# Performance work log

Measured on AMD Instinct MI355X. Metric: run time of the kernel, lower is better.

Reference implementation:

```python
import jax, jax.numpy as jnp
import numpy as np

NUM_BINS = 256
EPS = 1e-8


def setup_inputs() -> dict:
    key = jax.random.key(0)
    k1, k2 = jax.random.split(key)
    x = jax.random.uniform(k1, (4096, 8192), dtype=jnp.float32)
    y = jax.random.uniform(k2, (4096, 8192), dtype=jnp.float32)
    return {"x": x, "y": y}


def reference(x, y):
    # min-max normalize to [0, 1]
    xn = (x - jnp.min(x)) / (jnp.max(x) - jnp.min(x) + EPS)
    yn = (y - jnp.min(y)) / (jnp.max(y) - jnp.min(y) + EPS)
    # bin indices, clamped to [0, NUM_BINS-1] (floor(1.0*N) == N gets clipped)
    x_idx = jnp.clip(jnp.floor(xn * NUM_BINS).astype(jnp.int32), 0, NUM_BINS - 1)
    y_idx = jnp.clip(jnp.floor(yn * NUM_BINS).astype(jnp.int32), 0, NUM_BINS - 1)
    n = x.shape[0] * x.shape[1]
    # joint histogram via scatter-add on flattened (x_idx, y_idx) pairs
    flat = (x_idx * NUM_BINS + y_idx).reshape(-1)
    hist_xy = jnp.zeros((NUM_BINS * NUM_BINS,), jnp.float32).at[flat].add(1.0)
    hist_xy = hist_xy.reshape(NUM_BINS, NUM_BINS)
    p_xy = hist_xy / n
    p_x = jnp.sum(p_xy, axis=1)  # marginal over y
    p_y = jnp.sum(p_xy, axis=0)  # marginal over x
    # MI: sum over cells where p_xy>0 and both marginals>0
    px_py = p_x[:, None] * p_y[None, :]
    valid = (p_xy > 0) & (p_x[:, None] > 0) & (p_y[None, :] > 0)
    safe_pxy = jnp.where(valid, p_xy, 1.0)
    safe_den = jnp.where(valid, px_py, 1.0)
    mi = jnp.sum(jnp.where(valid, p_xy * jnp.log(safe_pxy / safe_den), 0.0))
    # normalized MI
    h_x = -jnp.sum(p_x * jnp.log(p_x + EPS))
    h_y = -jnp.sum(p_y * jnp.log(p_y + EPS))
    mi = mi / (jnp.sqrt(h_x * h_y) + EPS)
    return -mi
```

## Files before the change

kernel.cpp:

```cpp
#include <hip/hip_runtime.h>
#include <stdint.h>
#include <math.h>

#define HIST_BINS   65536
#define HIST_WORDS8 16384

typedef float f4 __attribute__((ext_vector_type(4)));

__device__ __forceinline__ f4 ldnt(const f4* p){ return __builtin_nontemporal_load(p); }

__device__ __forceinline__ uint32_t f2key(float f){
    uint32_t u = __float_as_uint(f);
    return (u & 0x80000000u) ? ~u : (u | 0x80000000u);
}
__device__ __forceinline__ float key2f(uint32_t k){
    uint32_t u = (k & 0x80000000u) ? (k ^ 0x80000000u) : ~k;
    return __uint_as_float(u);
}


__global__ void init_kernel(uint32_t* __restrict__ mm, uint32_t* __restrict__ csum){
    int t = threadIdx.x;
    if (t < 4) mm[t] = (t & 1) ? 0u : 0xFFFFFFFFu;
    csum[t] = 0u;
}

__device__ __forceinline__ void mm4(f4 a, float& mn, float& mx){
    mn = fminf(mn, fminf(fminf(a[0], a[1]), fminf(a[2], a[3])));
    mx = fmaxf(mx, fmaxf(fmaxf(a[0], a[1]), fmaxf(a[2], a[3])));
}

__global__ void __launch_bounds__(1024)
minmax_kernel(const f4* __restrict__ x, const f4* __restrict__ y,
              uint32_t* __restrict__ mm, int n4, int nblk_per){
    int isy = (blockIdx.x >= (unsigned)nblk_per) ? 1 : 0;
    const f4* __restrict__ src = isy ? y : x;
    int bid = blockIdx.x - isy * nblk_per;
    int seg = n4 / nblk_per;
    int base = bid * seg;
    const int chunk = 1024 * 8;
    float mn = INFINITY, mx = -INFINITY;
    int off = 0;
    for (; off + chunk <= seg; off += chunk){
        const f4* p = src + base + off + threadIdx.x;
        f4 v0 = p[0],        v1 = p[1024],     v2 = p[2 * 1024], v3 = p[3 * 1024];
        f4 v4 = p[4 * 1024], v5 = p[5 * 1024], v6 = p[6 * 1024], v7 = p[7 * 1024];
        mm4(v0, mn, mx); mm4(v1, mn, mx); mm4(v2, mn, mx); mm4(v3, mn, mx);
        mm4(v4, mn, mx); mm4(v5, mn, mx); mm4(v6, mn, mx); mm4(v7, mn, mx);
    }
    for (int i = base + off + threadIdx.x; i < base + seg; i += 1024) mm4(src[i], mn, mx);
    if (bid == nblk_per - 1)
        for (int i = nblk_per * seg + threadIdx.x; i < n4; i += 1024) mm4(src[i], mn, mx);

    #pragma unroll
    for (int o = 32; o > 0; o >>= 1){
        mn = fminf(mn, __shfl_down(mn, o, 64));
        mx = fmaxf(mx, __shfl_down(mx, o, 64));
    }
    __shared__ float smn[16], smx[16];
    int lane = threadIdx.x & 63, wid = threadIdx.x >> 6;
    if (lane == 0){ smn[wid] = mn; smx[wid] = mx; }
    __syncthreads();
    if (threadIdx.x == 0){
        for (int w = 1; w < 16; ++w){ mn = fminf(mn, smn[w]); mx = fmaxf(mx, smx[w]); }
        atomicMin(&mm[isy * 2 + 0], f2key(mn));
        atomicMax(&mm[isy * 2 + 1], f2key(mx));
    }
}

__device__ __forceinline__ void bin_pair(float vx, float vy,
                                         float mnx, float sx, float mny, float sy,
                                         uint32_t* lh){
    int ix = (int)floorf((vx - mnx) * sx);
    int iy = (int)floorf((vy - mny) * sy);
    ix = ix < 0 ? 0 : (ix > 255 ? 255 : ix);
    iy = iy < 0 ? 0 : (iy > 255 ? 255 : iy);
    uint32_t bin = ((uint32_t)ix << 8) | (uint32_t)iy;
    atomicAdd(&lh[bin >> 2], 1u << ((bin & 3u) * 8u));
}

__device__ __forceinline__ void bin4(f4 a, f4 b,
                                     float mnx, float sx, float mny, float sy,
                                     uint32_t* lh){
    bin_pair(a[0], b[0], mnx, sx, mny, sy, lh);
    bin_pair(a[1], b[1], mnx, sx, mny, sy, lh);
    bin_pair(a[2], b[2], mnx, sx, mny, sy, lh);
    bin_pair(a[3], b[3], mnx, sx, mny, sy, lh);
}

__global__ void __launch_bounds__(1024)
hist_kernel(const f4* __restrict__ x, const f4* __restrict__ y,
            const uint32_t* __restrict__ mm, uint32_t* __restrict__ out32,
            int n4, int atomic_flush){
    __shared__ uint32_t lh[HIST_WORDS8];
    for (int w = threadIdx.x; w < HIST_WORDS8; w += blockDim.x) lh[w] = 0u;
    __syncthreads();

    float mnx = key2f(mm[0]);
    float sx  = 256.0f / ((key2f(mm[1]) - mnx) + 1e-8f);
    float mny = key2f(mm[2]);
    float sy  = 256.0f / ((key2f(mm[3]) - mny) + 1e-8f);

    int seg  = n4 / gridDim.x;
    int base = blockIdx.x * seg;
    const int chunk = 1024 * 4;
    int off = 0;
    for (; off + chunk <= seg; off += chunk){
        const f4* px = x + base + off + threadIdx.x;
        const f4* py = y + base + off + threadIdx.x;
        f4 a0 = ldnt(px),            a1 = ldnt(px + 1024);
        f4 a2 = ldnt(px + 2 * 1024), a3 = ldnt(px + 3 * 1024);
        f4 b0 = ldnt(py),            b1 = ldnt(py + 1024);
        f4 b2 = ldnt(py + 2 * 1024), b3 = ldnt(py + 3 * 1024);
        bin4(a0, b0, mnx, sx, mny, sy, lh);
        bin4(a1, b1, mnx, sx, mny, sy, lh);
        bin4(a2, b2, mnx, sx, mny, sy, lh);
        bin4(a3, b3, mnx, sx, mny, sy, lh);
    }
    for (int i = base + off + threadIdx.x; i < base + seg; i += 1024)
        bin4(x[i], y[i], mnx, sx, mny, sy, lh);
    if (blockIdx.x == gridDim.x - 1)
        for (int i = gridDim.x * seg + threadIdx.x; i < n4; i += 1024)
            bin4(x[i], y[i], mnx, sx, mny, sy, lh);
    __syncthreads();

    if (!atomic_flush){
        uint32_t* part = out32 + (size_t)blockIdx.x * HIST_WORDS8;
        for (int w = threadIdx.x; w < HIST_WORDS8; w += blockDim.x) part[w] = lh[w];
    } else {
        for (int w = threadIdx.x; w < HIST_WORDS8; w += blockDim.x){
            uint32_t v = lh[w];
            if (v){
                uint32_t c0 = v & 255u, c1 = (v >> 8) & 255u, c2 = (v >> 16) & 255u, c3 = v >> 24;
                if (c0) atomicAdd(&out32[4*w + 0], c0);
                if (c1) atomicAdd(&out32[4*w + 1], c1);
                if (c2) atomicAdd(&out32[4*w + 2], c2);
                if (c3) atomicAdd(&out32[4*w + 3], c3);
            }
        }
    }
}

__global__ void __launch_bounds__(1024)
reduce_kernel(const uint32_t* __restrict__ partials, uint32_t* __restrict__ hist,
              uint32_t* __restrict__ rsum, uint32_t* __restrict__ csum, int nparts){
    __shared__ uint32_t sm[64][16][16];
    int t = threadIdx.x;
    int ql = t & 15, g = t >> 4;
    int per = nparts >> 6;
    uint32_t c[16];
    #pragma unroll
    for (int k = 0; k < 16; ++k) c[k] = 0;
    const uint4* base = (const uint4*)partials;
    size_t qoff = (size_t)blockIdx.x * 16 + ql;
    #pragma unroll 8
    for (int j = 0; j < per; ++j){
        uint4 v = base[(size_t)(g * per + j) * (HIST_WORDS8 / 4) + qoff];
        c[ 0] += v.x & 255u; c[ 1] += (v.x >> 8) & 255u; c[ 2] += (v.x >> 16) & 255u; c[ 3] += v.x >> 24;
        c[ 4] += v.y & 255u; c[ 5] += (v.y >> 8) & 255u; c[ 6] += (v.y >> 16) & 255u; c[ 7] += v.y >> 24;
        c[ 8] += v.z & 255u; c[ 9] += (v.z >> 8) & 255u; c[10] += (v.z >> 16) & 255u; c[11] += v.z >> 24;
        c[12] += v.w & 255u; c[13] += (v.w >> 8) & 255u; c[14] += (v.w >> 16) & 255u; c[15] += v.w >> 24;
    }
    #pragma unroll
    for (int k = 0; k < 16; ++k) sm[g][k][ql] = c[k];
    __syncthreads();
    uint32_t s = 0;
    if (t < 256){
        int q2 = t & 15;
        int k  = t >> 4;
        #pragma unroll 8
        for (int gg = 0; gg < 64; ++gg) s += sm[gg][k][q2];
        hist[(size_t)blockIdx.x * 256 + q2 * 16 + k] = s;
        atomicAdd(&csum[q2 * 16 + k], s);
    }
    __syncthreads();
    uint32_t* flat = &sm[0][0][0];
    if (t < 256){
        uint32_t bs = s;
        #pragma unroll
        for (int o = 32; o > 0; o >>= 1) bs += __shfl_down(bs, o, 64);
        if ((t & 63) == 0) flat[t >> 6] = bs;
    }
    __syncthreads();
    if (t == 0) rsum[blockIdx.x] = flat[0] + flat[1] + flat[2] + flat[3];
}

__device__ double bsum1024(double v, double* red, int t){
    #pragma unroll
    for (int o = 32; o > 0; o >>= 1) v += __shfl_down(v, o, 64);
    __syncthreads();
    if ((t & 63) == 0) red[t >> 6] = v;
    __syncthreads();
    if (t == 0){
        double s = 0.0;
        for (int w = 0; w < 16; ++w) s += red[w];
        v = s;
    }
    return v;
}

__global__ void __launch_bounds__(1024)
finalize_kernel(const uint32_t* __restrict__ hist,
                const uint32_t* __restrict__ rsum, const uint32_t* __restrict__ csum,
                float* __restrict__ out, int n, int marg){
    __shared__ uint32_t lrs[256], lcs[256];
    __shared__ uint32_t csum4[4][256];
    __shared__ double red[16];
    int t = threadIdx.x;

    if (!marg){
        if (t < 256){ lrs[t] = rsum[t]; lcs[t] = csum[t]; }
    } else {
        {
            int r = t >> 2, q = t & 3;
            const uint4* hp = (const uint4*)(hist + r * 256 + q * 64);
            uint32_t s = 0;
            #pragma unroll
            for (int k = 0; k < 16; ++k){ uint4 v = hp[k]; s += v.x + v.y + v.z + v.w; }
            s += __shfl_down(s, 2, 64);
            s += __shfl_down(s, 1, 64);
            if (q == 0) lrs[r] = s;
        }
        {
            int c = t & 255, g = t >> 8;
            const uint32_t* hp = hist + g * 64 * 256 + c;
            uint32_t s = 0;
            #pragma unroll 8
            for (int r = 0; r < 64; ++r) s += hp[r * 256];
            csum4[g][c] = s;
        }
        __syncthreads();
        if (t < 256) lcs[t] = csum4[0][t] + csum4[1][t] + csum4[2][t] + csum4[3][t];
    }
    __syncthreads();

    const double invn = 1.0 / (double)n;
    const double dn = (double)n;

    double mi = 0.0;
    {
        int q = t & 63, g = t >> 6;
        const uint4* h4 = (const uint4*)hist;
        for (int k = 0; k < 16; ++k){
            int r = g * 16 + k;
            uint4 v = h4[r * 64 + q];
            double rs = (double)lrs[r];
            uint32_t cc[4] = {v.x, v.y, v.z, v.w};
            #pragma unroll
            for (int j = 0; j < 4; ++j){
                if (cc[j]){
                    double ratio = ((double)cc[j] * dn) / (rs * (double)lcs[q * 4 + j]);
                    mi += (double)cc[j] * (double)logf((float)ratio);
                }
            }
        }
        mi *= invn;
    }
    double hx = 0.0, hy = 0.0;
    if (t < 256){
        double px = (double)lrs[t] * invn;
        double py = (double)lcs[t] * invn;
        hx = px * log(px + 1e-8);
        hy = py * log(py + 1e-8);
    }
    double mi_s = bsum1024(mi, red, t);
    double hx_s = bsum1024(hx, red, t);
    double hy_s = bsum1024(hy, red, t);
    if (t == 0){
        double h_x = -hx_s, h_y = -hy_s;
        double nmi = mi_s / (sqrt(h_x * h_y) + 1e-8);
        out[0] = (float)(-nmi);
    }
}

extern "C" void kernel_launch(void* const* d_in, const int* in_sizes, int n_in,
                              void* d_out, int out_size, void* d_ws, size_t ws_size,
                              hipStream_t stream){
    const f4* x = (const f4*)d_in[0];
    const f4* y = (const f4*)d_in[1];
    float* out = (float*)d_out;
    uint32_t* ws = (uint32_t*)d_ws;
    uint32_t* hist = ws;
    uint32_t* mm   = ws + HIST_BINS;
    uint32_t* rsum = ws + HIST_BINS + 64;
    uint32_t* csum = ws + HIST_BINS + 64 + 256;
    uint32_t* partials = ws + HIST_BINS + 64 + 512;

    int n  = in_sizes[0];
    int n4 = n / 4;

    size_t head = (size_t)HIST_BINS + 64 + 512;
    size_t need512 = (head + (size_t)512 * HIST_WORDS8) * 4;
    size_t need256 = (head + (size_t)256 * HIST_WORDS8) * 4;
    int nblk, atomic_flush;
    if (ws_size >= need512)      { nblk = 512; atomic_flush = 0; }
    else if (ws_size >= need256) { nblk = 256; atomic_flush = 0; }
    else                         { nblk = 512; atomic_flush = 1; }

    if (atomic_flush)
        hipMemsetAsync(hist, 0, HIST_BINS * sizeof(uint32_t), stream);
    init_kernel<<<1, 256, 0, stream>>>(mm, csum);
    minmax_kernel<<<512, 1024, 0, stream>>>(x, y, mm, n4, 256);
    hist_kernel<<<nblk, 1024, 0, stream>>>(x, y, mm,
                                           atomic_flush ? hist : partials, n4, atomic_flush);
    if (!atomic_flush)
        reduce_kernel<<<256, 1024, 0, stream>>>(partials, hist, rsum, csum, nblk);
    finalize_kernel<<<1, 1024, 0, stream>>>(hist, rsum, csum, out, n, atomic_flush);
}
```

Measured before the change: 371.3 us.

## Fuse reduce and finalize into cooperative kernel, drop init and atomic minmax

Per-block min/max results now go to slots and are reduced inside the histogram kernel, so the init kernel and the global atomics are gone. The reduce and finalize kernels merge into one cooperative kernel that uses grid syncs for the column sums and MI partials, which removes a single-block finalize pass over the full 65536-bin histogram. The change also switches the histogram loads from nontemporal to ordinary loads and vectorizes the partial-histogram write-out. In exchange it pays for a cooperative launch and two grid-wide barriers.

```diff
diff --git a/kernel.cpp b/kernel.cpp
--- a/kernel.cpp
+++ b/kernel.cpp
@@ -1,29 +1,14 @@
 #include <hip/hip_runtime.h>
+#include <hip/hip_cooperative_groups.h>
 #include <stdint.h>
 #include <math.h>
 
-#define HIST_BINS   65536
+namespace cg = cooperative_groups;
+
 #define HIST_WORDS8 16384
 
 typedef float f4 __attribute__((ext_vector_type(4)));
 
-__device__ __forceinline__ f4 ldnt(const f4* p){ return __builtin_nontemporal_load(p); }
-
-__device__ __forceinline__ uint32_t f2key(float f){
-    uint32_t u = __float_as_uint(f);
-    return (u & 0x80000000u) ? ~u : (u | 0x80000000u);
-}
-__device__ __forceinline__ float key2f(uint32_t k){
-    uint32_t u = (k & 0x80000000u) ? (k ^ 0x80000000u) : ~k;
-    return __uint_as_float(u);
-}
-
-
-__global__ void init_kernel(uint32_t* __restrict__ mm, uint32_t* __restrict__ csum){
-    int t = threadIdx.x;
-    if (t < 4) mm[t] = (t & 1) ? 0u : 0xFFFFFFFFu;
-    csum[t] = 0u;
-}
 
 __device__ __forceinline__ void mm4(f4 a, float& mn, float& mx){
     mn = fminf(mn, fminf(fminf(a[0], a[1]), fminf(a[2], a[3])));
@@ -32,7 +17,7 @@
 
 __global__ void __launch_bounds__(1024)
 minmax_kernel(const f4* __restrict__ x, const f4* __restrict__ y,
-              uint32_t* __restrict__ mm, int n4, int nblk_per){
+              float2* __restrict__ slots, int n4, int nblk_per){
     int isy = (blockIdx.x >= (unsigned)nblk_per) ? 1 : 0;
     const f4* __restrict__ src = isy ? y : x;
     int bid = blockIdx.x - isy * nblk_per;
@@ -63,8 +48,7 @@
     __syncthreads();
     if (threadIdx.x == 0){
         for (int w = 1; w < 16; ++w){ mn = fminf(mn, smn[w]); mx = fmaxf(mx, smx[w]); }
-        atomicMin(&mm[isy * 2 + 0], f2key(mn));
-        atomicMax(&mm[isy * 2 + 1], f2key(mx));
+        slots[blockIdx.x] = make_float2(mn, mx);
     }
 }
 
@@ -90,45 +74,73 @@
 
 __global__ void __launch_bounds__(1024)
 hist_kernel(const f4* __restrict__ x, const f4* __restrict__ y,
-            const uint32_t* __restrict__ mm, uint32_t* __restrict__ out32,
-            int n4, int atomic_flush){
+            const float2* __restrict__ slots, uint32_t* __restrict__ csum,
+            uint32_t* __restrict__ out32, int n4, int atomic_flush){
     __shared__ uint32_t lh[HIST_WORDS8];
-    for (int w = threadIdx.x; w < HIST_WORDS8; w += blockDim.x) lh[w] = 0u;
-    __syncthreads();
-
-    float mnx = key2f(mm[0]);
-    float sx  = 256.0f / ((key2f(mm[1]) - mnx) + 1e-8f);
-    float mny = key2f(mm[2]);
-    float sy  = 256.0f / ((key2f(mm[3]) - mny) + 1e-8f);
+    int t = threadIdx.x;
+    if (blockIdx.x == 0 && t < 256) csum[t] = 0u;
+
+    float mnx, sx, mny, sy;
+    {
+        float mn = INFINITY, mx = -INFINITY;
+        if (t < 512){ float2 s = slots[t]; mn = s.x; mx = s.y; }
+        #pragma unroll
+        for (int o = 32; o > 0; o >>= 1){
+            mn = fminf(mn, __shfl_down(mn, o, 64));
+            mx = fmaxf(mx, __shfl_down(mx, o, 64));
+        }
+        int lane = t & 63, wid = t >> 6;
+        if (lane == 0 && wid < 8){ lh[2*wid] = __float_as_uint(mn); lh[2*wid+1] = __float_as_uint(mx); }
+        __syncthreads();
+        if (t == 0){
+            float a = fminf(fminf(__uint_as_float(lh[0]),  __uint_as_float(lh[2])),
+                            fminf(__uint_as_float(lh[4]),  __uint_as_float(lh[6])));
+            float b = fmaxf(fmaxf(__uint_as_float(lh[1]),  __uint_as_float(lh[3])),
+                            fmaxf(__uint_as_float(lh[5]),  __uint_as_float(lh[7])));
+            float c = fminf(fminf(__uint_as_float(lh[8]),  __uint_as_float(lh[10])),
+                            fminf(__uint_as_float(lh[12]), __uint_as_float(lh[14])));
+            float d = fmaxf(fmaxf(__uint_as_float(lh[9]),  __uint_as_float(lh[11])),
+                            fmaxf(__uint_as_float(lh[13]), __uint_as_float(lh[15])));
+            lh[16] = __float_as_uint(a); lh[17] = __float_as_uint(b);
+            lh[18] = __float_as_uint(c); lh[19] = __float_as_uint(d);
+        }
+        __syncthreads();
+        mnx = __uint_as_float(lh[16]);
+        sx  = 256.0f / ((__uint_as_float(lh[17]) - mnx) + 1e-8f);
+        mny = __uint_as_float(lh[18]);
+        sy  = 256.0f / ((__uint_as_float(lh[19]) - mny) + 1e-8f);
+        __syncthreads();
+    }
+    for (int w = t; w < HIST_WORDS8; w += blockDim.x) lh[w] = 0u;
+    __syncthreads();
 
     int seg  = n4 / gridDim.x;
     int base = blockIdx.x * seg;
     const int chunk = 1024 * 4;
     int off = 0;
     for (; off + chunk <= seg; off += chunk){
-        const f4* px = x + base + off + threadIdx.x;
-        const f4* py = y + base + off + threadIdx.x;
-        f4 a0 = ldnt(px),            a1 = ldnt(px + 1024);
-        f4 a2 = ldnt(px + 2 * 1024), a3 = ldnt(px + 3 * 1024);
-        f4 b0 = ldnt(py),            b1 = ldnt(py + 1024);
-        f4 b2 = ldnt(py + 2 * 1024), b3 = ldnt(py + 3 * 1024);
+        const f4* px = x + base + off + t;
+        const f4* py = y + base + off + t;
+        f4 a0 = px[0],        a1 = px[1024], a2 = px[2 * 1024], a3 = px[3 * 1024];
+        f4 b0 = py[0],        b1 = py[1024], b2 = py[2 * 1024], b3 = py[3 * 1024];
         bin4(a0, b0, mnx, sx, mny, sy, lh);
         bin4(a1, b1, mnx, sx, mny, sy, lh);
         bin4(a2, b2, mnx, sx, mny, sy, lh);
         bin4(a3, b3, mnx, sx, mny, sy, lh);
     }
-    for (int i = base + off + threadIdx.x; i < base + seg; i += 1024)
+    for (int i = base + off + t; i < base + seg; i += 1024)
         bin4(x[i], y[i], mnx, sx, mny, sy, lh);
     if (blockIdx.x == gridDim.x - 1)
-        for (int i = gridDim.x * seg + threadIdx.x; i < n4; i += 1024)
+        for (int i = gridDim.x * seg + t; i < n4; i += 1024)
             bin4(x[i], y[i], mnx, sx, mny, sy, lh);
     __syncthreads();
 
     if (!atomic_flush){
-        uint32_t* part = out32 + (size_t)blockIdx.x * HIST_WORDS8;
-        for (int w = threadIdx.x; w < HIST_WORDS8; w += blockDim.x) part[w] = lh[w];
+        uint4* part = (uint4*)(out32 + (size_t)blockIdx.x * HIST_WORDS8);
+        const uint4* l4 = (const uint4*)lh;
+        for (int q = t; q < HIST_WORDS8 / 4; q += blockDim.x) part[q] = l4[q];
     } else {
-        for (int w = threadIdx.x; w < HIST_WORDS8; w += blockDim.x){
+        for (int w = t; w < HIST_WORDS8; w += blockDim.x){
             uint32_t v = lh[w];
             if (v){
                 uint32_t c0 = v & 255u, c1 = (v >> 8) & 255u, c2 = (v >> 16) & 255u, c3 = v >> 24;
@@ -142,134 +154,119 @@
 }
 
 __global__ void __launch_bounds__(1024)
-reduce_kernel(const uint32_t* __restrict__ partials, uint32_t* __restrict__ hist,
-              uint32_t* __restrict__ rsum, uint32_t* __restrict__ csum, int nparts){
+reduce_finalize_kernel(const uint32_t* __restrict__ partials,
+                       const uint32_t* __restrict__ ghist,
+                       uint32_t* __restrict__ csum,
+                       double* __restrict__ dslots,
+                       float* __restrict__ out, int n, int nparts){
+    cg::grid_group grid = cg::this_grid();
     __shared__ uint32_t sm[64][16][16];
+    uint32_t* flat = &sm[0][0][0];
+    uint32_t* lcs  = flat + 64;
+    double*  dred  = (double*)(flat + 512);
     int t = threadIdx.x;
-    int ql = t & 15, g = t >> 4;
-    int per = nparts >> 6;
-    uint32_t c[16];
-    #pragma unroll
-    for (int k = 0; k < 16; ++k) c[k] = 0;
-    const uint4* base = (const uint4*)partials;
-    size_t qoff = (size_t)blockIdx.x * 16 + ql;
-    #pragma unroll 8
-    for (int j = 0; j < per; ++j){
-        uint4 v = base[(size_t)(g * per + j) * (HIST_WORDS8 / 4) + qoff];
-        c[ 0] += v.x & 255u; c[ 1] += (v.x >> 8) & 255u; c[ 2] += (v.x >> 16) & 255u; c[ 3] += v.x >> 24;
-        c[ 4] += v.y & 255u; c[ 5] += (v.y >> 8) & 255u; c[ 6] += (v.y >> 16) & 255u; c[ 7] += v.y >> 24;
-        c[ 8] += v.z & 255u; c[ 9] += (v.z >> 8) & 255u; c[10] += (v.z >> 16) & 255u; c[11] += v.z >> 24;
-        c[12] += v.w & 255u; c[13] += (v.w >> 8) & 255u; c[14] += (v.w >> 16) & 255u; c[15] += v.w >> 24;
-    }
-    #pragma unroll
-    for (int k = 0; k < 16; ++k) sm[g][k][ql] = c[k];
-    __syncthreads();
-    uint32_t s = 0;
-    if (t < 256){
-        int q2 = t & 15;
-        int k  = t >> 4;
-        #pragma unroll 8
-        for (int gg = 0; gg < 64; ++gg) s += sm[gg][k][q2];
-        hist[(size_t)blockIdx.x * 256 + q2 * 16 + k] = s;
-        atomicAdd(&csum[q2 * 16 + k], s);
-    }
-    __syncthreads();
-    uint32_t* flat = &sm[0][0][0];
-    if (t < 256){
-        uint32_t bs = s;
+    int b = blockIdx.x;
+    int col = ((t & 15) << 4) | (t >> 4);
+    uint32_t cnt = 0;
+
+    if (nparts > 0){
+        int ql = t & 15, g = t >> 4;
+        int per = nparts >> 6;
+        uint32_t c[16];
         #pragma unroll
-        for (int o = 32; o > 0; o >>= 1) bs += __shfl_down(bs, o, 64);
-        if ((t & 63) == 0) flat[t >> 6] = bs;
-    }
-    __syncthreads();
-    if (t == 0) rsum[blockIdx.x] = flat[0] + flat[1] + flat[2] + flat[3];
-}
-
-__device__ double bsum1024(double v, double* red, int t){
-    #pragma unroll
-    for (int o = 32; o > 0; o >>= 1) v += __shfl_down(v, o, 64);
-    __syncthreads();
-    if ((t & 63) == 0) red[t >> 6] = v;
-    __syncthreads();
-    if (t == 0){
-        double s = 0.0;
-        for (int w = 0; w < 16; ++w) s += red[w];
-        v = s;
-    }
-    return v;
-}
-
-__global__ void __launch_bounds__(1024)
-finalize_kernel(const uint32_t* __restrict__ hist,
-                const uint32_t* __restrict__ rsum, const uint32_t* __restrict__ csum,
-                float* __restrict__ out, int n, int marg){
-    __shared__ uint32_t lrs[256], lcs[256];
-    __shared__ uint32_t csum4[4][256];
-    __shared__ double red[16];
-    int t = threadIdx.x;
-
-    if (!marg){
-        if (t < 256){ lrs[t] = rsum[t]; lcs[t] = csum[t]; }
-    } else {
-        {
-            int r = t >> 2, q = t & 3;
-            const uint4* hp = (const uint4*)(hist + r * 256 + q * 64);
-            uint32_t s = 0;
-            #pragma unroll
-            for (int k = 0; k < 16; ++k){ uint4 v = hp[k]; s += v.x + v.y + v.z + v.w; }
-            s += __shfl_down(s, 2, 64);
-            s += __shfl_down(s, 1, 64);
-            if (q == 0) lrs[r] = s;
-        }
-        {
-            int c = t & 255, g = t >> 8;
-            const uint32_t* hp = hist + g * 64 * 256 + c;
+        for (int k = 0; k < 16; ++k) c[k] = 0;
+        const uint4* base4 = (const uint4*)partials;
+        size_t qoff = (size_t)b * 16 + ql;
+        for (int j = 0; j < per; ++j){
+            uint4 v = base4[(size_t)(g * per + j) * (HIST_WORDS8 / 4) + qoff];
+            c[ 0] += v.x & 255u; c[ 1] += (v.x >> 8) & 255u; c[ 2] += (v.x >> 16) & 255u; c[ 3] += v.x >> 24;
+            c[ 4] += v.y & 255u; c[ 5] += (v.y >> 8) & 255u; c[ 6] += (v.y >> 16) & 255u; c[ 7] += v.y >> 24;
+            c[ 8] += v.z & 255u; c[ 9] += (v.z >> 8) & 255u; c[10] += (v.z >> 16) & 255u; c[11] += v.z >> 24;
+            c[12] += v.w & 255u; c[13] += (v.w >> 8) & 255u; c[14] += (v.w >> 16) & 255u; c[15] += v.w >> 24;
+        }
+        #pragma unroll
+        for (int k = 0; k < 16; ++k) sm[g][k][ql] = c[k];
+        __syncthreads();
+        if (t < 256){
+            int q2 = t & 15, k = t >> 4;
             uint32_t s = 0;
             #pragma unroll 8
-            for (int r = 0; r < 64; ++r) s += hp[r * 256];
-            csum4[g][c] = s;
-        }
-        __syncthreads();
-        if (t < 256) lcs[t] = csum4[0][t] + csum4[1][t] + csum4[2][t] + csum4[3][t];
-    }
-    __syncthreads();
-
-    const double invn = 1.0 / (double)n;
-    const double dn = (double)n;
-
+            for (int gg = 0; gg < 64; ++gg) s += sm[gg][k][q2];
+            cnt = s;
+        }
+    } else {
+        if (t < 256) cnt = ghist[b * 256 + col];
+    }
+    __syncthreads();
+
+    uint32_t r = cnt;
+    #pragma unroll
+    for (int o = 32; o > 0; o >>= 1) r += __shfl_down(r, o, 64);
+    if ((t & 63) == 0) flat[t >> 6] = r;
+    __syncthreads();
+    uint32_t rsum_b = 0;
+    #pragma unroll
+    for (int w = 0; w < 16; ++w) rsum_b += flat[w];
+
+    if (t < 256) atomicAdd(&csum[col], cnt);
+    grid.sync();
+
+    if (t < 256) lcs[t] = __hip_atomic_load(&csum[t], __ATOMIC_RELAXED, __HIP_MEMORY_SCOPE_AGENT);
+    __syncthreads();
+
+    const double invn = 1.0 / (double)n, dn = (double)n;
     double mi = 0.0;
-    {
-        int q = t & 63, g = t >> 6;
-        const uint4* h4 = (const uint4*)hist;
-        for (int k = 0; k < 16; ++k){
-            int r = g * 16 + k;
-            uint4 v = h4[r * 64 + q];
-            double rs = (double)lrs[r];
-            uint32_t cc[4] = {v.x, v.y, v.z, v.w};
-            #pragma unroll
-            for (int j = 0; j < 4; ++j){
-                if (cc[j]){
-                    double ratio = ((double)cc[j] * dn) / (rs * (double)lcs[q * 4 + j]);
-                    mi += (double)cc[j] * (double)logf((float)ratio);
-                }
+    if (t < 256 && cnt){
+        double ratio = ((double)cnt * dn) / ((double)rsum_b * (double)lcs[col]);
+        mi = (double)cnt * (double)logf((float)ratio);
+    }
+    #pragma unroll
+    for (int o = 32; o > 0; o >>= 1) mi += __shfl_down(mi, o, 64);
+    if ((t & 63) == 0) dred[t >> 6] = mi;
+    __syncthreads();
+    if (t == 0){
+        double mis = 0.0;
+        for (int w = 0; w < 16; ++w) mis += dred[w];
+        mis *= invn;
+        double px = (double)rsum_b * invn;
+        double hx = px * log(px + 1e-8);
+        double py = (double)lcs[b] * invn;
+        double hy = py * log(py + 1e-8);
+        __hip_atomic_store(&dslots[3*b+0], mis, __ATOMIC_RELAXED, __HIP_MEMORY_SCOPE_AGENT);
+        __hip_atomic_store(&dslots[3*b+1], hx,  __ATOMIC_RELAXED, __HIP_MEMORY_SCOPE_AGENT);
+        __hip_atomic_store(&dslots[3*b+2], hy,  __ATOMIC_RELAXED, __HIP_MEMORY_SCOPE_AGENT);
+    }
+    grid.sync();
+
+    if (b == 0){
+        double vmi = 0.0, vhx = 0.0, vhy = 0.0;
+        if (t < 256){
+            vmi = __hip_atomic_load(&dslots[3*t+0], __ATOMIC_RELAXED, __HIP_MEMORY_SCOPE_AGENT);
+            vhx = __hip_atomic_load(&dslots[3*t+1], __ATOMIC_RELAXED, __HIP_MEMORY_SCOPE_AGENT);
+            vhy = __hip_atomic_load(&dslots[3*t+2], __ATOMIC_RELAXED, __HIP_MEMORY_SCOPE_AGENT);
+        }
+        #pragma unroll
+        for (int o = 32; o > 0; o >>= 1){
+            vmi += __shfl_down(vmi, o, 64);
+            vhx += __shfl_down(vhx, o, 64);
+            vhy += __shfl_down(vhy, o, 64);
+        }
+        __syncthreads();
+        if ((t & 63) == 0){
+            dred[t >> 6]      = vmi;
+            dred[16 + (t >> 6)] = vhx;
+            dred[32 + (t >> 6)] = vhy;
+        }
+        __syncthreads();
+        if (t == 0){
+            double mi_s = 0.0, hx_s = 0.0, hy_s = 0.0;
+            for (int w = 0; w < 16; ++w){
+                mi_s += dred[w]; hx_s += dred[16 + w]; hy_s += dred[32 + w];
             }
-        }
-        mi *= invn;
-    }
-    double hx = 0.0, hy = 0.0;
-    if (t < 256){
-        double px = (double)lrs[t] * invn;
-        double py = (double)lcs[t] * invn;
-        hx = px * log(px + 1e-8);
-        hy = py * log(py + 1e-8);
-    }
-    double mi_s = bsum1024(mi, red, t);
-    double hx_s = bsum1024(hx, red, t);
-    double hy_s = bsum1024(hy, red, t);
-    if (t == 0){
-        double h_x = -hx_s, h_y = -hy_s;
-        double nmi = mi_s / (sqrt(h_x * h_y) + 1e-8);
-        out[0] = (float)(-nmi);
+            double h_x = -hx_s, h_y = -hy_s;
+            double nmi = mi_s / (sqrt(h_x * h_y) + 1e-8);
+            out[0] = (float)(-nmi);
+        }
     }
 }
 
@@ -280,30 +277,31 @@
     const f4* y = (const f4*)d_in[1];
     float* out = (float*)d_out;
     uint32_t* ws = (uint32_t*)d_ws;
-    uint32_t* hist = ws;
-    uint32_t* mm   = ws + HIST_BINS;
-    uint32_t* rsum = ws + HIST_BINS + 64;
-    uint32_t* csum = ws + HIST_BINS + 64 + 256;
-    uint32_t* partials = ws + HIST_BINS + 64 + 512;
+    float2*   slots  = (float2*)ws;
+    uint32_t* csum   = ws + 1024;
+    double*   dslots = (double*)(ws + 1280);
+    uint32_t* ghist  = ws + 4096;
+    uint32_t* partials = ws + 4096;
 
     int n  = in_sizes[0];
     int n4 = n / 4;
 
-    size_t head = (size_t)HIST_BINS + 64 + 512;
-    size_t need512 = (head + (size_t)512 * HIST_WORDS8) * 4;
-    size_t need256 = (head + (size_t)256 * HIST_WORDS8) * 4;
-    int nblk, atomic_flush;
-    if (ws_size >= need512)      { nblk = 512; atomic_flush = 0; }
-    else if (ws_size >= need256) { nblk = 256; atomic_flush = 0; }
-    else                         { nblk = 512; atomic_flush = 1; }
+    size_t need512 = ((size_t)4096 + (size_t)512 * HIST_WORDS8) * 4;
+    size_t need256 = ((size_t)4096 + (size_t)256 * HIST_WORDS8) * 4;
+    int nblk, atomic_flush, nparts;
+    if (ws_size >= need512)      { nblk = 512; atomic_flush = 0; nparts = 512; }
+    else if (ws_size >= need256) { nblk = 256; atomic_flush = 0; nparts = 256; }
+    else                         { nblk = 512; atomic_flush = 1; nparts = 0;   }
 
     if (atomic_flush)
-        hipMemsetAsync(hist, 0, HIST_BINS * sizeof(uint32_t), stream);
-    init_kernel<<<1, 256, 0, stream>>>(mm, csum);
-    minmax_kernel<<<512, 1024, 0, stream>>>(x, y, mm, n4, 256);
-    hist_kernel<<<nblk, 1024, 0, stream>>>(x, y, mm,
-                                           atomic_flush ? hist : partials, n4, atomic_flush);
-    if (!atomic_flush)
-        reduce_kernel<<<256, 1024, 0, stream>>>(partials, hist, rsum, csum, nblk);
-    finalize_kernel<<<1, 1024, 0, stream>>>(hist, rsum, csum, out, n, atomic_flush);
-}
+        hipMemsetAsync(ghist, 0, 65536 * sizeof(uint32_t), stream);
+    minmax_kernel<<<512, 1024, 0, stream>>>(x, y, slots, n4, 256);
+    hist_kernel<<<nblk, 1024, 0, stream>>>(x, y, slots, csum,
+                                           atomic_flush ? ghist : partials, n4, atomic_flush);
+    const uint32_t* pp = partials;
+    const uint32_t* gh = ghist;
+    void* args[] = { (void*)&pp, (void*)&gh, (void*)&csum, (void*)&dslots,
+                     (void*)&out, (void*)&n, (void*)&nparts };
+    hipLaunchCooperativeKernel((const void*)reduce_finalize_kernel,
+                               dim3(256), dim3(1024), args, 0, stream);
+}
```

Result: slower. 406.8 us (+9.6%).
